# Optimization experiments

Measured on AMD Instinct MI355X. Metric: run time of the kernel, lower is better.

Reference implementation:

```python
import jax, jax.numpy as jnp
import numpy as np

D_MODEL = 2048
N_HEADS = 16
D_HEAD = 128
B = 2
S = 2048


def setup_inputs() -> dict:
    key = jax.random.key(0)
    ks = jax.random.split(key, 9)
    sc_in = 1.0 / np.sqrt(D_MODEL)
    sc_hd = 1.0 / np.sqrt(N_HEADS * D_HEAD)
    return {
        "x": jax.random.normal(ks[0], (B, S, D_MODEL), dtype=jnp.float32),
        "Wq": jax.random.normal(ks[1], (D_MODEL, N_HEADS * D_HEAD), dtype=jnp.float32) * sc_in,
        "bq": jax.random.normal(ks[2], (N_HEADS * D_HEAD,), dtype=jnp.float32) * 0.01,
        "Wk": jax.random.normal(ks[3], (D_MODEL, N_HEADS * D_HEAD), dtype=jnp.float32) * sc_in,
        "bk": jax.random.normal(ks[4], (N_HEADS * D_HEAD,), dtype=jnp.float32) * 0.01,
        "Wv": jax.random.normal(ks[5], (D_MODEL, N_HEADS * D_HEAD), dtype=jnp.float32) * sc_in,
        "bv": jax.random.normal(ks[6], (N_HEADS * D_HEAD,), dtype=jnp.float32) * 0.01,
        "Wo": jax.random.normal(ks[7], (N_HEADS * D_HEAD, D_MODEL), dtype=jnp.float32) * sc_hd,
        "bo": jax.random.normal(ks[8], (D_MODEL,), dtype=jnp.float32) * 0.01,
    }


def reference(x, Wq, bq, Wk, bk, Wv, bv, Wo, bo):
    b, s, _ = x.shape
    # projections -> [b, s, h, d] -> [b, h, s, d]
    q = (x @ Wq + bq).reshape(b, s, N_HEADS, D_HEAD).transpose(0, 2, 1, 3)
    k = (x @ Wk + bk).reshape(b, s, N_HEADS, D_HEAD).transpose(0, 2, 1, 3)
    v = (x @ Wv + bv).reshape(b, s, N_HEADS, D_HEAD).transpose(0, 2, 1, 3)
    scale = 1.0 / jnp.sqrt(jnp.asarray(D_HEAD, dtype=x.dtype))
    scores = jnp.einsum("bhsd,bhtd->bhst", q, k) * scale  # [b,h,s,s]
    causal = jnp.triu(jnp.ones((s, s), dtype=bool), k=1)
    scores = jnp.where(causal, jnp.asarray(-jnp.inf, dtype=scores.dtype), scores)
    attn = jax.nn.softmax(scores, axis=-1)
    ctx = jnp.einsum("bhst,bhtd->bhsd", attn, v)  # [b,h,s,d]
    ctx = ctx.transpose(0, 2, 1, 3).reshape(b, s, N_HEADS * D_HEAD)
    return ctx @ Wo + bo
```

## Files before the change

kernel.cpp:

```cpp
#include <hip/hip_runtime.h>
#include <hip/hip_bf16.h>
#include <stdint.h>

#define S_LEN  2048
#define DMODEL 2048
#define NHEADS 16
#define DHEAD  128
#define NBATCH 2
#define MROWS  (NBATCH * S_LEN)

typedef __bf16 bf16_t;
typedef __bf16 bf16x8 __attribute__((ext_vector_type(8)));
typedef float  f32x4  __attribute__((ext_vector_type(4)));
typedef float  f32x16 __attribute__((ext_vector_type(16)));

#define MFMA_BF16(A, B, C) __builtin_amdgcn_mfma_f32_16x16x32_bf16((A), (B), (C), 0, 0, 0)
#define MFMA32(A, B, C)    __builtin_amdgcn_mfma_f32_32x32x16_bf16((A), (B), (C), 0, 0, 0)

__device__ __forceinline__ void gload_lds16(const void* g, void* l) {
  __builtin_amdgcn_global_load_lds(
      (__attribute__((address_space(1))) uint32_t*)(uintptr_t)g,
      (__attribute__((address_space(3))) uint32_t*)l,
      16, 0, 0);
}

__device__ __forceinline__ unsigned pk2(float lo, float hi) {
  const unsigned short a = __builtin_bit_cast(unsigned short, (bf16_t)lo);
  const unsigned short b = __builtin_bit_cast(unsigned short, (bf16_t)hi);
  return (unsigned)a | ((unsigned)b << 16);
}

__global__ __launch_bounds__(256) void prep_kernel(
    const float* __restrict__ X, bf16_t* __restrict__ Xb,
    const float* __restrict__ W0, const float* __restrict__ W1,
    const float* __restrict__ W2, const float* __restrict__ W3,
    bf16_t* __restrict__ T0, bf16_t* __restrict__ T1,
    bf16_t* __restrict__ T2, bf16_t* __restrict__ T3) {
  const int bid = blockIdx.x;
  if (bid >= 4096) {
    const int i = (bid - 4096) * 256 + threadIdx.x;
    const f32x4 a = ((const f32x4*)X)[2 * i];
    const f32x4 b = ((const f32x4*)X)[2 * i + 1];
    bf16x8 o;
#pragma unroll
    for (int j = 0; j < 4; ++j) { o[j] = (bf16_t)a[j]; o[j + 4] = (bf16_t)b[j]; }
    ((bf16x8*)Xb)[i] = o;
    return;
  }
  const int wz  = bid >> 10;
  const int rem = bid & 1023;
  const float* W; bf16_t* T;
  switch (wz) {
    case 0:  W = W0; T = T0; break;
    case 1:  W = W1; T = T1; break;
    case 2:  W = W2; T = T2; break;
    default: W = W3; T = T3; break;
  }
  __shared__ float tile[64][65];
  const int r0 = (rem >> 5) * 64;
  const int c0 = (rem & 31) * 64;
  const int tx = threadIdx.x & 63;
  const int ty = threadIdx.x >> 6;
#pragma unroll
  for (int i = 0; i < 16; ++i) {
    const int r = ty + i * 4;
    tile[r][tx] = W[(size_t)(r0 + r) * DMODEL + c0 + tx];
  }
  __syncthreads();
#pragma unroll
  for (int i = 0; i < 16; ++i) {
    const int r = ty + i * 4;
    T[(size_t)(c0 + r) * DMODEL + r0 + tx] = (bf16_t)tile[tx][r];
  }
}

__device__ __forceinline__ void gemm8_body(const bf16_t* __restrict__ A,
                                           const bf16_t* __restrict__ Bt,
                                           const float* __restrict__ bias,
                                           void* __restrict__ out,
                                           int m0, int n0, int mode) {
  __shared__ __align__(16) char lds8[2 * 49152];
  const int tid  = threadIdx.x;
  const int lane = tid & 63;
  const int w    = tid >> 6;
  const int g    = lane >> 4;
  const int l16  = lane & 15;
  const int wm   = w >> 2;
  const int wn   = w & 3;

  f32x4 acc[4][4];
#pragma unroll
  for (int i = 0; i < 4; ++i)
#pragma unroll
    for (int j = 0; j < 4; ++j) acc[i][j] = (f32x4){0.f, 0.f, 0.f, 0.f};

  const int st_r0 = tid >> 3;
  const int st_ch = tid & 7;

  auto stage = [&](int tile, int r) {
    if (tile >= DMODEL / 64) return;
    const int kt = tile << 6;
    char* db = lds8 + (tile & 1) * 49152 + r * 16384 + w * 1024;
    const bf16_t* sb = (r == 0) ? (A + (size_t)m0 * DMODEL + kt)
                                : (Bt + (size_t)(n0 + ((r - 1) << 7)) * DMODEL + kt);
#pragma unroll
    for (int jj = 0; jj < 2; ++jj) {
      const int row = jj * 64 + st_r0;
      gload_lds16(sb + (size_t)row * DMODEL + ((st_ch ^ (row & 7)) << 3),
                  db + jj * 8192);
    }
  };

  stage(0, 0); stage(0, 1); stage(0, 2); stage(1, 0);
  asm volatile("s_waitcnt vmcnt(2)" ::: "memory");
  __builtin_amdgcn_s_barrier();

#pragma unroll 2
  for (int t = 0; t < DMODEL / 64; ++t) {
    const char* cb = lds8 + (t & 1) * 49152;
    bf16x8 af[4][2], b0[2][2], b1[2][2];
#pragma unroll
    for (int i = 0; i < 4; ++i) {
      const int row = wm * 64 + i * 16 + l16;
      const char* rp = cb + row * 128;
#pragma unroll
      for (int ks = 0; ks < 2; ++ks)
        af[i][ks] = *(const bf16x8*)(rp + ((((ks << 2) | g) ^ (row & 7)) << 4));
    }
#pragma unroll
    for (int j = 0; j < 2; ++j) {
      const int row = (wn & 1) * 64 + j * 16 + l16;
      const char* rp = cb + 16384 + (wn >> 1) * 16384 + row * 128;
#pragma unroll
      for (int ks = 0; ks < 2; ++ks)
        b0[j][ks] = *(const bf16x8*)(rp + ((((ks << 2) | g) ^ (row & 7)) << 4));
    }
    stage(t + 1, 1); stage(t + 1, 2);
    __builtin_amdgcn_s_barrier();
    asm volatile("s_waitcnt lgkmcnt(0)" ::: "memory");
#pragma unroll
    for (int i = 0; i < 4; ++i)
#pragma unroll
      for (int j = 0; j < 2; ++j) {
        acc[i][j] = MFMA_BF16(af[i][0], b0[j][0], acc[i][j]);
        acc[i][j] = MFMA_BF16(af[i][1], b0[j][1], acc[i][j]);
      }
    __builtin_amdgcn_s_barrier();
#pragma unroll
    for (int j = 0; j < 2; ++j) {
      const int row = (wn & 1) * 64 + (j + 2) * 16 + l16;
      const char* rp = cb + 16384 + (wn >> 1) * 16384 + row * 128;
#pragma unroll
      for (int ks = 0; ks < 2; ++ks)
        b1[j][ks] = *(const bf16x8*)(rp + ((((ks << 2) | g) ^ (row & 7)) << 4));
    }
    stage(t + 2, 0);
    __builtin_amdgcn_s_barrier();
    asm volatile("s_waitcnt lgkmcnt(0)" ::: "memory");
#pragma unroll
    for (int i = 0; i < 4; ++i)
#pragma unroll
      for (int j = 0; j < 2; ++j) {
        acc[i][j + 2] = MFMA_BF16(af[i][0], b1[j][0], acc[i][j + 2]);
        acc[i][j + 2] = MFMA_BF16(af[i][1], b1[j][1], acc[i][j + 2]);
      }
    if (t < DMODEL / 64 - 2) asm volatile("s_waitcnt vmcnt(2)" ::: "memory");
    else                     asm volatile("s_waitcnt vmcnt(0)" ::: "memory");
    __builtin_amdgcn_s_barrier();
  }

  if (mode == 2) {
    bf16_t* tr = (bf16_t*)lds8;
#pragma unroll
    for (int i = 0; i < 4; ++i) {
#pragma unroll
      for (int j = 0; j < 4; ++j) {
        const int nl = wn * 64 + j * 16 + l16;
        const int ml = wm * 64 + i * 16 + g * 4;
        const float bb = bias[n0 + nl];
        union { unsigned short u[4]; uint64_t v; } pk;
#pragma unroll
        for (int r = 0; r < 4; ++r)
          pk.u[r] = __builtin_bit_cast(unsigned short, (bf16_t)(acc[i][j][r] + bb));
        *(uint64_t*)&tr[nl * 136 + ml] = pk.v;
      }
    }
    __syncthreads();
    const int b = m0 >> 11;
    const int s0 = m0 & (S_LEN - 1);
#pragma unroll
    for (int it = 0; it < 8; ++it) {
      const int c   = it * 512 + tid;
      const int nl  = c >> 4;
      const int ml8 = c & 15;
      const bf16x8 v = *(const bf16x8*)&tr[nl * 136 + ml8 * 8];
      const int n  = n0 + nl;
      const int h  = n >> 7, dd = n & (DHEAD - 1);
      *(bf16x8*)((bf16_t*)out +
                 ((size_t)(b * NHEADS + h) * DHEAD + dd) * S_LEN + s0 + ml8 * 8) = v;
    }
    return;
  }

#pragma unroll
  for (int i = 0; i < 4; ++i) {
#pragma unroll
    for (int j = 0; j < 4; ++j) {
      const int n    = n0 + wn * 64 + j * 16 + l16;
      const float bb = bias[n];
#pragma unroll
      for (int r = 0; r < 4; ++r) {
        const int m   = m0 + wm * 64 + i * 16 + g * 4 + r;
        const float v = acc[i][j][r] + bb;
        if (mode == 0) {
          const int b = m >> 11, s = m & (S_LEN - 1);
          const int h = n >> 7,  d = n & (DHEAD - 1);
          ((bf16_t*)out)[((size_t)(b * NHEADS + h) * S_LEN + s) * DHEAD + d] = (bf16_t)v;
        } else {
          ((float*)out)[(size_t)m * DMODEL + n] = v;
        }
      }
    }
  }
}

__global__ __launch_bounds__(512, 2) void gemm_qkv(
    const bf16_t* __restrict__ Xb,
    const bf16_t* __restrict__ WqT, const bf16_t* __restrict__ WkT,
    const bf16_t* __restrict__ WvT,
    const float* __restrict__ bq, const float* __restrict__ bk,
    const float* __restrict__ bv,
    bf16_t* __restrict__ Qg, bf16_t* __restrict__ Kg, bf16_t* __restrict__ VTg) {
  const int bid = blockIdx.x;
  const int wg  = (bid & 7) * 96 + (bid >> 3);
  const int x   = wg & 7;
  const int y   = (wg >> 3) & 31;
  const int z0  = wg >> 8;
  const bf16_t* Bt  = (z0 == 0) ? WqT : (z0 == 1) ? WkT : WvT;
  const float* bias = (z0 == 0) ? bq  : (z0 == 1) ? bk  : bv;
  void* out         = (z0 == 0) ? (void*)Qg : (z0 == 1) ? (void*)Kg : (void*)VTg;
  gemm8_body(Xb, Bt, bias, out, y * 128, x * 256, (z0 == 2) ? 2 : 0);
}

__global__ __launch_bounds__(512, 2) void gemm_out(
    const bf16_t* __restrict__ Ctx, const bf16_t* __restrict__ WoT,
    const float* __restrict__ bo, float* __restrict__ out) {
  gemm8_body(Ctx, WoT, bo, out, blockIdx.y * 128, blockIdx.x * 256, 1);
}

#define KTILE_B 16384
#define VTILE_B 16384
#define ABUF_B  (KTILE_B + VTILE_B)

__global__ __launch_bounds__(256, 2) void attn_kernel(
    const bf16_t* __restrict__ Qg, const bf16_t* __restrict__ Kg,
    const bf16_t* __restrict__ VTg, bf16_t* __restrict__ ctx) {
  __shared__ __align__(16) char ldsbuf[2][ABUF_B];
  __shared__ float lbuf[4][32];

  const int tid  = threadIdx.x;
  const int lane = tid & 63;
  const int w    = tid >> 6;
  const int l31  = lane & 31;
  const int hi   = lane >> 5;

  const int id   = blockIdx.x;
  const int bh   = id & 31;
  const int jraw = id >> 5;
  const int j    = (jraw < 8) ? jraw : 23 - jraw;
  const int q0   = j * 128;
  const int qw   = q0 + w * 32;
  const int tq   = (qw + 31) >> 6;
  const int NT   = (q0 + 128) >> 6;

  const size_t bho = (size_t)bh * S_LEN * DHEAD;
  const bf16_t* Qb  = Qg + bho;
  const bf16_t* Kb  = Kg + bho;
  const bf16_t* VTb = VTg + bho;

  auto stageT = [&](int t) {
    const int kt = t << 6;
    char* dst = ldsbuf[t & 1];
#pragma unroll
    for (int i = 0; i < 4; ++i) {
      const int c   = i * 256 + tid;
      const int row = c >> 4, ch = c & 15;
      gload_lds16(Kb + (size_t)(kt + row) * DHEAD + ((ch ^ (row & 7)) << 3),
                  dst + (i * 256 + (tid & ~63)) * 16);
    }
#pragma unroll
    for (int i = 0; i < 4; ++i) {
      const int c   = i * 256 + tid;
      const int row = c >> 3, ch = c & 7;
      gload_lds16(VTb + (size_t)row * S_LEN + kt + ((ch ^ (row & 7)) << 3),
                  dst + KTILE_B + (i * 256 + (tid & ~63)) * 16);
    }
  };

  bf16x8 qreg[8];
#pragma unroll
  for (int s = 0; s < 8; ++s)
    qreg[s] = *(const bf16x8*)(Qb + (size_t)(qw + l31) * DHEAD + s * 16 + hi * 8);

  f32x16 oacc[4];
#pragma unroll
  for (int d0 = 0; d0 < 4; ++d0)
#pragma unroll
    for (int e = 0; e < 16; ++e) oacc[d0][e] = 0.f;

  float m = -1e30f, lsum = 0.f;
  const float sc2 = 0.12751751135f;

  stageT(0);
  asm volatile("s_waitcnt vmcnt(0)" ::: "memory");
  __syncthreads();

  for (int t = 0; t < NT; ++t) {
    const char* bK = ldsbuf[t & 1];
    const char* bV = bK + KTILE_B;
    if (t + 1 < NT) stageT(t + 1);

    if (t <= tq) {
      const int kt = t << 6;
      f32x16 stt[2];
#pragma unroll
      for (int kh = 0; kh < 2; ++kh)
#pragma unroll
        for (int e = 0; e < 16; ++e) stt[kh][e] = 0.f;
#pragma unroll
      for (int kh = 0; kh < 2; ++kh) {
        const int row = kh * 32 + l31;
        const char* rb = bK + row * 256;
        const int swz = (row & 7) << 4;
#pragma unroll
        for (int s = 0; s < 8; ++s) {
          const bf16x8 kf = *(const bf16x8*)(rb + ((((s << 1) | hi) << 4) ^ swz));
          stt[kh] = MFMA32(kf, qreg[s], stt[kh]);
        }
      }
      if (t == tq) {
        const int qg = qw + l31;
#pragma unroll
        for (int kh = 0; kh < 2; ++kh)
#pragma unroll
          for (int r = 0; r < 16; ++r) {
            const int kv = kt + kh * 32 + (r & 3) + 8 * (r >> 2) + 4 * hi;
            stt[kh][r] = (kv > qg) ? -1e30f : stt[kh][r];
          }
      }
      float pm = fmaxf(stt[0][0], stt[1][0]);
#pragma unroll
      for (int r = 1; r < 16; ++r)
        pm = fmaxf(pm, fmaxf(stt[0][r], stt[1][r]));
      pm = fmaxf(pm, __shfl_xor(pm, 32));
      const float pmax = pm * sc2;
      if (!__all(pmax <= m + 8.f)) {
        const float mn   = fmaxf(m, pmax);
        const float corr = __builtin_amdgcn_exp2f(m - mn);
        m = mn;
        lsum *= corr;
        if (!hi) lbuf[w][l31] = corr;
#pragma unroll
        for (int r = 0; r < 16; ++r) {
          const float cr = lbuf[w][(r & 3) + 8 * (r >> 2) + 4 * hi];
#pragma unroll
          for (int d0 = 0; d0 < 4; ++d0) oacc[d0][r] *= cr;
        }
      }
      float rs = 0.f;
#pragma unroll
      for (int kh = 0; kh < 2; ++kh)
#pragma unroll
        for (int r = 0; r < 16; ++r) {
          const float p = __builtin_amdgcn_exp2f(__builtin_fmaf(stt[kh][r], sc2, -m));
          stt[kh][r] = p;
          rs += p;
        }
      rs += __shfl_xor(rs, 32);
      lsum += rs;
      unsigned pw_[2][8];
#pragma unroll
      for (int kh = 0; kh < 2; ++kh)
#pragma unroll
        for (int jj = 0; jj < 8; ++jj)
          pw_[kh][jj] = pk2(stt[kh][2 * jj], stt[kh][2 * jj + 1]);
      bf16x8 pa[4];
#pragma unroll
      for (int kh = 0; kh < 2; ++kh)
#pragma unroll
        for (int c2 = 0; c2 < 2; ++c2) {
          const unsigned o0 = pw_[kh][4 * c2 + 0], o1 = pw_[kh][4 * c2 + 1];
          const unsigned o2 = pw_[kh][4 * c2 + 2], o3 = pw_[kh][4 * c2 + 3];
          const unsigned p0 = (unsigned)__shfl_xor((int)o0, 32);
          const unsigned p1 = (unsigned)__shfl_xor((int)o1, 32);
          const unsigned p2 = (unsigned)__shfl_xor((int)o2, 32);
          const unsigned p3 = (unsigned)__shfl_xor((int)o3, 32);
          union { unsigned u[4]; bf16x8 v; } uu;
          uu.u[0] = hi ? p2 : o0;
          uu.u[1] = hi ? p3 : o1;
          uu.u[2] = hi ? o2 : p0;
          uu.u[3] = hi ? o3 : p1;
          pa[2 * kh + c2] = uu.v;
        }
#pragma unroll
      for (int d0 = 0; d0 < 4; ++d0) {
        const int row = d0 * 32 + l31;
        const char* rb = bV + row * 128;
        const int swz = (row & 7) << 4;
#pragma unroll
        for (int ks = 0; ks < 4; ++ks) {
          const bf16x8 vb = *(const bf16x8*)(rb + ((((ks << 1) | hi) << 4) ^ swz));
          oacc[d0] = MFMA32(pa[ks], vb, oacc[d0]);
        }
      }
    }
    asm volatile("s_waitcnt vmcnt(0)" ::: "memory");
    __syncthreads();
  }

  if (!hi) lbuf[w][l31] = 1.0f / lsum;
  const int b = bh >> 4, h = bh & 15;
#pragma unroll
  for (int r = 0; r < 16; ++r) {
    const int cro = (r & 3) + 8 * (r >> 2) + 4 * hi;
    const float li = lbuf[w][cro];
    const size_t base = ((size_t)(b * S_LEN + qw + cro)) * DMODEL + h * DHEAD;
#pragma unroll
    for (int d0 = 0; d0 < 4; ++d0)
      ctx[base + d0 * 32 + l31] = (bf16_t)(oacc[d0][r] * li);
  }
}

extern "C" void kernel_launch(void* const* d_in, const int* in_sizes, int n_in,
                              void* d_out, int out_size, void* d_ws, size_t ws_size,
                              hipStream_t stream) {
  const float* x  = (const float*)d_in[0];
  const float* Wq = (const float*)d_in[1];
  const float* bq = (const float*)d_in[2];
  const float* Wk = (const float*)d_in[3];
  const float* bk = (const float*)d_in[4];
  const float* Wv = (const float*)d_in[5];
  const float* bv = (const float*)d_in[6];
  const float* Wo = (const float*)d_in[7];
  const float* bo = (const float*)d_in[8];

  char* ws = (char*)d_ws;
  const size_t MB = 1ull << 20;
  bf16_t* Xb  = (bf16_t*)(ws + 0);
  bf16_t* WqT = (bf16_t*)(ws + 16 * MB);
  bf16_t* WkT = (bf16_t*)(ws + 24 * MB);
  bf16_t* WvT = (bf16_t*)(ws + 32 * MB);
  bf16_t* WoT = (bf16_t*)(ws + 40 * MB);
  bf16_t* Qg  = (bf16_t*)(ws + 48 * MB);
  bf16_t* Kg  = (bf16_t*)(ws + 64 * MB);
  bf16_t* VTg = (bf16_t*)(ws + 80 * MB);
  bf16_t* Ctx = (bf16_t*)(ws + 96 * MB);
  if (ws_size < 112 * MB) return;

  prep_kernel<<<dim3(8192), 256, 0, stream>>>(x, Xb, Wq, Wk, Wv, Wo,
                                              WqT, WkT, WvT, WoT);
  gemm_qkv<<<dim3(768), 512, 0, stream>>>(
      Xb, WqT, WkT, WvT, bq, bk, bv, Qg, Kg, VTg);
  attn_kernel<<<dim3(512), 256, 0, stream>>>(Qg, Kg, VTg, Ctx);
  gemm_out<<<dim3(DMODEL / 256, MROWS / 128), 512, 0, stream>>>(Ctx, WoT, bo, (float*)d_out);
}
```

Baseline: 216.8 us.

## Split QKV GEMM into 64-row tiles, drop mid-loop barriers, add MFMA priority

Gives the QKV projection its own kernel with a 64x256 tile and a two-stage LDS buffer, doubling the grid to 1536 blocks and targeting four blocks per CU. The aim is better occupancy and wave balance across CUs, at the cost of lower data reuse per tile. It also removes two intermediate s_barriers in the output GEMM main loop. In the attention kernel, the MFMA sections are wrapped in s_setprio raises so matrix work is favoured over other waves. Removing those barriers risks races on the LDS buffers if the remaining waits are not enough to order the tile reuse.

```diff
diff --git a/kernel.cpp b/kernel.cpp
--- a/kernel.cpp
+++ b/kernel.cpp
@@ -74,11 +74,173 @@
   }
 }
 
+__global__ __launch_bounds__(512, 4) void gemm_qkv(
+    const bf16_t* __restrict__ Xb,
+    const bf16_t* __restrict__ WqT, const bf16_t* __restrict__ WkT,
+    const bf16_t* __restrict__ WvT,
+    const float* __restrict__ bq, const float* __restrict__ bk,
+    const float* __restrict__ bv,
+    bf16_t* __restrict__ Qg, bf16_t* __restrict__ Kg, bf16_t* __restrict__ VTg) {
+  __shared__ __align__(16) char lds[2 * 40960];
+  const int tid  = threadIdx.x;
+  const int lane = tid & 63;
+  const int w    = tid >> 6;
+  const int g    = lane >> 4;
+  const int l16  = lane & 15;
+  const int wm   = w >> 2;
+  const int wn   = w & 3;
+  const int NT   = DMODEL / 64;
+
+  const int bid = blockIdx.x;
+  const int wg  = (bid & 7) * 192 + (bid >> 3);
+  const int y   = wg & 63;
+  const int xz  = wg >> 6;
+  const int x   = xz & 7;
+  const int z0  = xz >> 3;
+  const int m0  = y * 64;
+  const int n0  = x * 256;
+  const bf16_t* Bt  = (z0 == 0) ? WqT : (z0 == 1) ? WkT : WvT;
+  const float* bias = (z0 == 0) ? bq  : (z0 == 1) ? bk  : bv;
+
+  f32x4 acc[2][4];
+#pragma unroll
+  for (int i = 0; i < 2; ++i)
+#pragma unroll
+    for (int j = 0; j < 4; ++j) acc[i][j] = (f32x4){0.f, 0.f, 0.f, 0.f};
+
+  auto stageA = [&](int tile) {
+    if (tile >= NT) return;
+    const int kt  = tile << 6;
+    const int row = tid >> 3, ch = tid & 7;
+    gload_lds16(Xb + (size_t)(m0 + row) * DMODEL + kt + ((ch ^ (row & 7)) << 3),
+                lds + (tile & 1) * 40960 + (tid & ~63) * 16);
+  };
+  auto stageB = [&](int tile, int h) {
+    if (tile >= NT) return;
+    const int kt = tile << 6;
+    char* db = lds + (tile & 1) * 40960 + 8192 + h * 16384;
+    const bf16_t* sb = Bt + (size_t)(n0 + h * 128) * DMODEL + kt;
+#pragma unroll
+    for (int jj = 0; jj < 2; ++jj) {
+      const int c   = jj * 512 + tid;
+      const int row = c >> 3, ch = c & 7;
+      gload_lds16(sb + (size_t)row * DMODEL + ((ch ^ (row & 7)) << 3),
+                  db + (jj * 512 + (tid & ~63)) * 16);
+    }
+  };
+
+  stageA(0); stageB(0, 0); stageB(0, 1); stageA(1);
+  asm volatile("s_waitcnt vmcnt(1)" ::: "memory");
+  __builtin_amdgcn_s_barrier();
+
+#pragma unroll 2
+  for (int t = 0; t < NT; ++t) {
+    const char* cbA = lds + (t & 1) * 40960;
+    const char* cbB = cbA + 8192;
+    bf16x8 af[2][2], b0[2][2], b1[2][2];
+#pragma unroll
+    for (int i = 0; i < 2; ++i) {
+      const int row = wm * 32 + i * 16 + l16;
+      const char* rp = cbA + row * 128;
+#pragma unroll
+      for (int ks = 0; ks < 2; ++ks)
+        af[i][ks] = *(const bf16x8*)(rp + ((((ks << 2) | g) ^ (row & 7)) << 4));
+    }
+#pragma unroll
+    for (int j = 0; j < 2; ++j) {
+      const int row = wn * 64 + j * 16 + l16;
+      const char* rp = cbB + row * 128;
+#pragma unroll
+      for (int ks = 0; ks < 2; ++ks)
+        b0[j][ks] = *(const bf16x8*)(rp + ((((ks << 2) | g) ^ (row & 7)) << 4));
+    }
+    stageB(t + 1, 0); stageB(t + 1, 1);
+    asm volatile("s_waitcnt lgkmcnt(0)" ::: "memory");
+#pragma unroll
+    for (int i = 0; i < 2; ++i)
+#pragma unroll
+      for (int j = 0; j < 2; ++j) {
+        acc[i][j] = MFMA_BF16(af[i][0], b0[j][0], acc[i][j]);
+        acc[i][j] = MFMA_BF16(af[i][1], b0[j][1], acc[i][j]);
+      }
+    __builtin_amdgcn_s_barrier();
+#pragma unroll
+    for (int j = 0; j < 2; ++j) {
+      const int row = wn * 64 + (j + 2) * 16 + l16;
+      const char* rp = cbB + row * 128;
+#pragma unroll
+      for (int ks = 0; ks < 2; ++ks)
+        b1[j][ks] = *(const bf16x8*)(rp + ((((ks << 2) | g) ^ (row & 7)) << 4));
+    }
+    stageA(t + 2);
+    asm volatile("s_waitcnt lgkmcnt(0)" ::: "memory");
+#pragma unroll
+    for (int i = 0; i < 2; ++i)
+#pragma unroll
+      for (int j = 0; j < 2; ++j) {
+        acc[i][j + 2] = MFMA_BF16(af[i][0], b1[j][0], acc[i][j + 2]);
+        acc[i][j + 2] = MFMA_BF16(af[i][1], b1[j][1], acc[i][j + 2]);
+      }
+    if (t < NT - 2) asm volatile("s_waitcnt vmcnt(1)" ::: "memory");
+    else            asm volatile("s_waitcnt vmcnt(0)" ::: "memory");
+    __builtin_amdgcn_s_barrier();
+  }
+
+  const int b  = m0 >> 11;
+  if (z0 == 2) {
+    bf16_t* tr = (bf16_t*)lds;
+#pragma unroll
+    for (int i = 0; i < 2; ++i) {
+#pragma unroll
+      for (int j = 0; j < 4; ++j) {
+        const int nl = wn * 64 + j * 16 + l16;
+        const int ml = wm * 32 + i * 16 + g * 4;
+        const float bb = bias[n0 + nl];
+        union { unsigned short u[4]; uint64_t v; } pk;
+#pragma unroll
+        for (int r = 0; r < 4; ++r)
+          pk.u[r] = __builtin_bit_cast(unsigned short, (bf16_t)(acc[i][j][r] + bb));
+        *(uint64_t*)&tr[nl * 72 + ml] = pk.v;
+      }
+    }
+    __syncthreads();
+    const int s0 = m0 & (S_LEN - 1);
+#pragma unroll
+    for (int it = 0; it < 4; ++it) {
+      const int c   = it * 512 + tid;
+      const int nl  = c >> 3;
+      const int ml8 = c & 7;
+      const bf16x8 v = *(const bf16x8*)&tr[nl * 72 + ml8 * 8];
+      const int n  = n0 + nl;
+      const int h  = n >> 7, dd = n & (DHEAD - 1);
+      *(bf16x8*)(VTg + ((size_t)(b * NHEADS + h) * DHEAD + dd) * S_LEN + s0 + ml8 * 8) = v;
+    }
+    return;
+  }
+  bf16_t* outb = (z0 == 0) ? Qg : Kg;
+#pragma unroll
+  for (int i = 0; i < 2; ++i) {
+#pragma unroll
+    for (int j = 0; j < 4; ++j) {
+      const int n    = n0 + wn * 64 + j * 16 + l16;
+      const float bb = bias[n];
+      const int h = n >> 7, d = n & (DHEAD - 1);
+#pragma unroll
+      for (int r = 0; r < 4; ++r) {
+        const int m = m0 + wm * 32 + i * 16 + g * 4 + r;
+        const int s = m & (S_LEN - 1);
+        outb[((size_t)(b * NHEADS + h) * S_LEN + s) * DHEAD + d] =
+            (bf16_t)(acc[i][j][r] + bb);
+      }
+    }
+  }
+}
+
 __device__ __forceinline__ void gemm8_body(const bf16_t* __restrict__ A,
                                            const bf16_t* __restrict__ Bt,
                                            const float* __restrict__ bias,
-                                           void* __restrict__ out,
-                                           int m0, int n0, int mode) {
+                                           float* __restrict__ out,
+                                           int m0, int n0) {
   __shared__ __align__(16) char lds8[2 * 49152];
   const int tid  = threadIdx.x;
   const int lane = tid & 63;
@@ -136,7 +298,6 @@
         b0[j][ks] = *(const bf16x8*)(rp + ((((ks << 2) | g) ^ (row & 7)) << 4));
     }
     stage(t + 1, 1); stage(t + 1, 2);
-    __builtin_amdgcn_s_barrier();
     asm volatile("s_waitcnt lgkmcnt(0)" ::: "memory");
 #pragma unroll
     for (int i = 0; i < 4; ++i)
@@ -155,7 +316,6 @@
         b1[j][ks] = *(const bf16x8*)(rp + ((((ks << 2) | g) ^ (row & 7)) << 4));
     }
     stage(t + 2, 0);
-    __builtin_amdgcn_s_barrier();
     asm volatile("s_waitcnt lgkmcnt(0)" ::: "memory");
 #pragma unroll
     for (int i = 0; i < 4; ++i)
@@ -169,39 +329,6 @@
     __builtin_amdgcn_s_barrier();
   }
 
-  if (mode == 2) {
-    bf16_t* tr = (bf16_t*)lds8;
-#pragma unroll
-    for (int i = 0; i < 4; ++i) {
-#pragma unroll
-      for (int j = 0; j < 4; ++j) {
-        const int nl = wn * 64 + j * 16 + l16;
-        const int ml = wm * 64 + i * 16 + g * 4;
-        const float bb = bias[n0 + nl];
-        union { unsigned short u[4]; uint64_t v; } pk;
-#pragma unroll
-        for (int r = 0; r < 4; ++r)
-          pk.u[r] = __builtin_bit_cast(unsigned short, (bf16_t)(acc[i][j][r] + bb));
-        *(uint64_t*)&tr[nl * 136 + ml] = pk.v;
-      }
-    }
-    __syncthreads();
-    const int b = m0 >> 11;
-    const int s0 = m0 & (S_LEN - 1);
-#pragma unroll
-    for (int it = 0; it < 8; ++it) {
-      const int c   = it * 512 + tid;
-      const int nl  = c >> 4;
-      const int ml8 = c & 15;
-      const bf16x8 v = *(const bf16x8*)&tr[nl * 136 + ml8 * 8];
-      const int n  = n0 + nl;
-      const int h  = n >> 7, dd = n & (DHEAD - 1);
-      *(bf16x8*)((bf16_t*)out +
-                 ((size_t)(b * NHEADS + h) * DHEAD + dd) * S_LEN + s0 + ml8 * 8) = v;
-    }
-    return;
-  }
-
 #pragma unroll
   for (int i = 0; i < 4; ++i) {
 #pragma unroll
@@ -210,42 +337,17 @@
       const float bb = bias[n];
 #pragma unroll
       for (int r = 0; r < 4; ++r) {
-        const int m   = m0 + wm * 64 + i * 16 + g * 4 + r;
-        const float v = acc[i][j][r] + bb;
-        if (mode == 0) {
-          const int b = m >> 11, s = m & (S_LEN - 1);
-          const int h = n >> 7,  d = n & (DHEAD - 1);
-          ((bf16_t*)out)[((size_t)(b * NHEADS + h) * S_LEN + s) * DHEAD + d] = (bf16_t)v;
-        } else {
-          ((float*)out)[(size_t)m * DMODEL + n] = v;
-        }
-      }
-    }
-  }
-}
-
-__global__ __launch_bounds__(512, 2) void gemm_qkv(
-    const bf16_t* __restrict__ Xb,
-    const bf16_t* __restrict__ WqT, const bf16_t* __restrict__ WkT,
-    const bf16_t* __restrict__ WvT,
-    const float* __restrict__ bq, const float* __restrict__ bk,
-    const float* __restrict__ bv,
-    bf16_t* __restrict__ Qg, bf16_t* __restrict__ Kg, bf16_t* __restrict__ VTg) {
-  const int bid = blockIdx.x;
-  const int wg  = (bid & 7) * 96 + (bid >> 3);
-  const int x   = wg & 7;
-  const int y   = (wg >> 3) & 31;
-  const int z0  = wg >> 8;
-  const bf16_t* Bt  = (z0 == 0) ? WqT : (z0 == 1) ? WkT : WvT;
-  const float* bias = (z0 == 0) ? bq  : (z0 == 1) ? bk  : bv;
-  void* out         = (z0 == 0) ? (void*)Qg : (z0 == 1) ? (void*)Kg : (void*)VTg;
-  gemm8_body(Xb, Bt, bias, out, y * 128, x * 256, (z0 == 2) ? 2 : 0);
+        const int m = m0 + wm * 64 + i * 16 + g * 4 + r;
+        out[(size_t)m * DMODEL + n] = acc[i][j][r] + bb;
+      }
+    }
+  }
 }
 
 __global__ __launch_bounds__(512, 2) void gemm_out(
     const bf16_t* __restrict__ Ctx, const bf16_t* __restrict__ WoT,
     const float* __restrict__ bo, float* __restrict__ out) {
-  gemm8_body(Ctx, WoT, bo, out, blockIdx.y * 128, blockIdx.x * 256, 1);
+  gemm8_body(Ctx, WoT, bo, out, blockIdx.y * 128, blockIdx.x * 256);
 }
 
 #define KTILE_B 16384
@@ -327,6 +429,7 @@
       for (int kh = 0; kh < 2; ++kh)
 #pragma unroll
         for (int e = 0; e < 16; ++e) stt[kh][e] = 0.f;
+      __builtin_amdgcn_s_setprio(1);
 #pragma unroll
       for (int kh = 0; kh < 2; ++kh) {
         const int row = kh * 32 + l31;
@@ -338,6 +441,7 @@
           stt[kh] = MFMA32(kf, qreg[s], stt[kh]);
         }
       }
+      __builtin_amdgcn_s_setprio(0);
       if (t == tq) {
         const int qg = qw + l31;
 #pragma unroll
@@ -402,6 +506,7 @@
           uu.u[3] = hi ? o3 : p1;
           pa[2 * kh + c2] = uu.v;
         }
+      __builtin_amdgcn_s_setprio(1);
 #pragma unroll
       for (int d0 = 0; d0 < 4; ++d0) {
         const int row = d0 * 32 + l31;
@@ -413,6 +518,7 @@
           oacc[d0] = MFMA32(pa[ks], vb, oacc[d0]);
         }
       }
+      __builtin_amdgcn_s_setprio(0);
     }
     asm volatile("s_waitcnt vmcnt(0)" ::: "memory");
     __syncthreads();
@@ -459,7 +565,7 @@
 
   prep_kernel<<<dim3(8192), 256, 0, stream>>>(x, Xb, Wq, Wk, Wv, Wo,
                                               WqT, WkT, WvT, WoT);
-  gemm_qkv<<<dim3(768), 512, 0, stream>>>(
+  gemm_qkv<<<dim3(1536), 512, 0, stream>>>(
       Xb, WqT, WkT, WvT, bq, bk, bv, Qg, Kg, VTg);
   attn_kernel<<<dim3(512), 256, 0, stream>>>(Qg, Kg, VTg, Ctx);
   gemm_out<<<dim3(DMODEL / 256, MROWS / 128), 512, 0, stream>>>(Ctx, WoT, bo, (float*)d_out);
```

Measured after the change: 235.3 us. 1.09x slower.
